# Kernel tuning notes

Measured on AMD Instinct MI355X. Metric: run time of the kernel, lower is better.

## Reference

```python
import jax, jax.numpy as jnp
import numpy as np

N = 65536      # num drones/nodes
E = 262144     # num directed edges
HID = 128      # hidden_dim
HEADS = 8      # gat1 heads
EPS = 1e-5


def _bn(x, g, b):
    # BatchNorm1d in training mode: batch statistics over dim 0 (biased var)
    mu = x.mean(0)
    var = ((x - mu) ** 2).mean(0)
    return (x - mu) * jax.lax.rsqrt(var + EPS) * g + b


def _gat(x, src, dst, W, a_src, a_dst, bias, heads, out_c, n, concat):
    # PyG GATConv math (self-loops already included in src/dst)
    xw = (x @ W).reshape(n, heads, out_c)               # [N,H,C]
    al_s = (xw * a_src).sum(-1)                          # [N,H]
    al_d = (xw * a_dst).sum(-1)                          # [N,H]
    e = jax.nn.leaky_relu(al_s[src] + al_d[dst], 0.2)    # [E',H]
    m = jax.ops.segment_max(e, dst, num_segments=n)      # stable softmax per target
    ex = jnp.exp(e - m[dst])
    den = jax.ops.segment_sum(ex, dst, num_segments=n)
    alpha = ex / den[dst]                                # [E',H]
    out = jax.ops.segment_sum(xw[src] * alpha[:, :, None], dst, num_segments=n)
    out = out.reshape(n, heads * out_c) if concat else out.mean(axis=1)
    return out + bias


def setup_inputs() -> dict:
    key = jax.random.key(0)
    ks = jax.random.split(key, 24)
    s = 0.05
    inp = {
        'node_features': jax.random.normal(ks[0], (N, HID), jnp.float32),
        'relative_poses': jax.random.normal(ks[1], (E, 6), jnp.float32),
        'pe_w1': jax.random.normal(ks[2], (6, 64), jnp.float32) * s,
        'pe_b1': jnp.zeros((64,), jnp.float32),
        'pe_g1': jnp.ones((64,), jnp.float32),
        'pe_be1': jnp.zeros((64,), jnp.float32),
        'pe_w2': jax.random.normal(ks[3], (64, HID), jnp.float32) * s,
        'pe_b2': jnp.zeros((HID,), jnp.float32),
        'pe_g2': jnp.ones((HID,), jnp.float32),
        'pe_be2': jnp.zeros((HID,), jnp.float32),
        'gamma_w': jax.random.normal(ks[4], (HID, HID), jnp.float32) * s,
        'gamma_b': jnp.zeros((HID,), jnp.float32),
        'beta_w': jax.random.normal(ks[5], (HID, HID), jnp.float32) * s,
        'beta_b': jnp.zeros((HID,), jnp.float32),
        'g1_w': jax.random.normal(ks[6], (HID, HEADS * HID), jnp.float32) * s,
        'g1_as': jax.random.normal(ks[7], (HEADS, HID), jnp.float32) * s,
        'g1_ad': jax.random.normal(ks[8], (HEADS, HID), jnp.float32) * s,
        'g1_b': jnp.zeros((HEADS * HID,), jnp.float32),
        'g2_w': jax.random.normal(ks[9], (HEADS * HID, HID), jnp.float32) * s,
        'g2_as': jax.random.normal(ks[10], (1, HID), jnp.float32) * s,
        'g2_ad': jax.random.normal(ks[11], (1, HID), jnp.float32) * s,
        'g2_b': jnp.zeros((HID,), jnp.float32),
        'edge_index': jax.random.randint(ks[12], (2, E), 0, N, jnp.int32),
    }
    return inp


def reference(node_features, relative_poses, pe_w1, pe_b1, pe_g1, pe_be1,
              pe_w2, pe_b2, pe_g2, pe_be2, gamma_w, gamma_b, beta_w, beta_b,
              g1_w, g1_as, g1_ad, g1_b, g2_w, g2_as, g2_ad, g2_b, edge_index):
    src, dst = edge_index[0], edge_index[1]
    # SpatialEncoding: pose MLP with training-mode BN, then FiLM modulation
    h = jax.nn.relu(_bn(relative_poses @ pe_w1 + pe_b1, pe_g1, pe_be1))
    h = jax.nn.relu(_bn(h @ pe_w2 + pe_b2, pe_g2, pe_be2))
    gamma = jax.nn.sigmoid(h @ gamma_w + gamma_b) * 2.0   # [E,HID]
    beta = h @ beta_w + beta_b
    modulated = gamma * node_features[src] + beta          # [E,HID]
    last = jnp.full((N,), -1, jnp.int32).at[dst].max(jnp.arange(E, dtype=jnp.int32))
    enc = jnp.where((last >= 0)[:, None], modulated[jnp.clip(last, 0)], node_features)
    # add self loops (PyG GATConv default)
    loops = jnp.arange(N, dtype=src.dtype)
    src_a = jnp.concatenate([src, loops])
    dst_a = jnp.concatenate([dst, loops])
    x = jax.nn.elu(_gat(enc, src_a, dst_a, g1_w, g1_as, g1_ad, g1_b, HEADS, HID, N, True))
    # dropout is identity in eval mode
    out = _gat(x, src_a, dst_a, g2_w, g2_as, g2_ad, g2_b, 1, HID, N, False)
    return out
```

## Files before the change

kernel.cpp:

```cpp
#include <hip/hip_runtime.h>
#include <hip/hip_bf16.h>
#include <math.h>

#define NN 65536
#define EE 262144

typedef unsigned short u16;
typedef unsigned int u32;
typedef __attribute__((ext_vector_type(8))) short bf16x8;
typedef __attribute__((ext_vector_type(4))) float f32x4;

__device__ __forceinline__ float bfu2f(u16 u){ return __uint_as_float(((u32)u)<<16); }
__device__ __forceinline__ u16 f2bfu(float f){
  u32 x = __float_as_uint(f);
  return (u16)((x + 0x7fffu + ((x>>16)&1u)) >> 16);
}
__device__ __forceinline__ float lrelu(float x){ return x>0.f ? x : 0.2f*x; }
__device__ __forceinline__ float fexp(float x){ return __expf(x); }

__global__ void k_cvtT(const float* __restrict__ B, u16* __restrict__ Bt, int K, int N){
  int idx = blockIdx.x*256+threadIdx.x;
  if (idx < K*N){ int k = idx/N, n = idx - k*N; Bt[n*K+k] = f2bfu(B[idx]); }
}

__global__ void k_cvtn(const float* __restrict__ nf, u16* __restrict__ nfb){
  int i = (blockIdx.x*256+threadIdx.x)*4;
  float4 v = *(const float4*)(nf + i);
  ushort4 o; o.x=f2bfu(v.x); o.y=f2bfu(v.y); o.z=f2bfu(v.z); o.w=f2bfu(v.w);
  *(ushort4*)(nfb + i) = o;
}

__global__ void k_bn1_stats(const float* __restrict__ poses, const float* __restrict__ w1,
                            const float* __restrict__ b1, float* __restrict__ sum1, float* __restrict__ sq1){
  int wave = (blockIdx.x*blockDim.x + threadIdx.x)>>6;
  int c = threadIdx.x & 63;
  float wc[6];
#pragma unroll
  for (int j=0;j<6;++j) wc[j] = w1[j*64+c];
  float bb = b1[c];
  float s=0.f,q=0.f;
  int e0 = wave*(EE/1024);
  for (int e=e0;e<e0+(EE/1024);++e){
    float z = bb;
#pragma unroll
    for (int j=0;j<6;++j) z = fmaf(poses[e*6+j], wc[j], z);
    s += z; q += z*z;
  }
  unsafeAtomicAdd(&sum1[c], s);
  unsafeAtomicAdd(&sq1[c], q);
}

__global__ void k_bn_fin(const float* __restrict__ sum, const float* __restrict__ sq,
                         const float* __restrict__ g, const float* __restrict__ be,
                         const float* __restrict__ bias0,
                         float* __restrict__ a, float* __restrict__ cc, int cols){
  int c = threadIdx.x;
  if (c<cols){
    float mu = sum[c]*(1.f/EE);
    float var = sq[c]*(1.f/EE) - mu*mu;
    float istd = rsqrtf(var + 1e-5f);
    float ac = istd*g[c];
    a[c] = ac;
    float cv = be[c] - mu*ac;
    if (bias0) cv += bias0[c]*ac;
    cc[c] = cv;
  }
}

__global__ void k_red2(const float* __restrict__ psum, const float* __restrict__ psq,
                       float* __restrict__ part2){
  int t = threadIdx.x;
  int b0 = blockIdx.x*128;
  float s = 0.f;
  if (t < 128){
    for (int k=0;k<128;++k) s += psum[(size_t)(b0+k)*128 + t];
  } else {
    int c = t-128;
    for (int k=0;k<128;++k) s += psq[(size_t)(b0+k)*128 + c];
  }
  part2[blockIdx.x*256 + t] = s;
}

__global__ void k_bn_fin2(const float* __restrict__ part2,
                          const float* __restrict__ g, const float* __restrict__ be,
                          const float* __restrict__ bias0,
                          float* __restrict__ a, float* __restrict__ cc){
  int c = threadIdx.x;
  if (c<128){
    float s=0.f,q=0.f;
    for (int k=0;k<32;++k){ s += part2[k*256+c]; q += part2[k*256+128+c]; }
    float mu = s*(1.f/EE);
    float var = q*(1.f/EE) - mu*mu;
    float istd = rsqrtf(var + 1e-5f);
    float ac = istd*g[c];
    a[c] = ac;
    cc[c] = be[c] - mu*ac + bias0[c]*ac;
  }
}

__global__ void k_h1(const float* __restrict__ poses, const float* __restrict__ w1, const float* __restrict__ b1,
                     const float* __restrict__ a1, const float* __restrict__ c1, u16* __restrict__ h1){
  int idx = blockIdx.x*256+threadIdx.x;
  int e = idx>>6, c = idx&63;
  float z = b1[c];
#pragma unroll
  for (int j=0;j<6;++j) z = fmaf(poses[e*6+j], w1[j*64+c], z);
  float h = z*a1[c]+c1[c];
  h1[idx] = f2bfu(h>0.f?h:0.f);
}

template<int EPI>
__launch_bounds__(256)
__global__ void k_mm(const u16* __restrict__ A, const u16* __restrict__ Bt,
                     const u16* __restrict__ Bt2,
                     int K, int lda, int ldbt, int ldc,
                     u16* __restrict__ outb,
                     const float* __restrict__ bias, const float* __restrict__ bias2,
                     float* __restrict__ ssum, float* __restrict__ ssq,
                     const float* __restrict__ gb,
                     const float* __restrict__ bb, const u16* __restrict__ nfselb,
                     const int* __restrict__ lastE){
  const int m0 = blockIdx.x*64, n0 = blockIdx.y*128;
  const int t = threadIdx.x;
  const int lane = t & 63, wv = t>>6;
  const int wr = wv>>1, wc = wv&1;
  __shared__ u16 Als[64*64];
  __shared__ u16 Bls[128*64];
  __shared__ u16 B2ls[EPI==7 ? 128*64 : 8];
  __shared__ float epiS[128][2];
  __shared__ float epiD[128][2];
  f32x4 acc[2][4];
  f32x4 acc2[2][4];
#pragma unroll
  for (int i=0;i<2;++i)
#pragma unroll
    for (int j=0;j<4;++j){ acc[i][j] = (f32x4){0.f,0.f,0.f,0.f}; acc2[i][j] = (f32x4){0.f,0.f,0.f,0.f}; }

  for (int k0=0;k0<K;k0+=64){
    constexpr int NS = (EPI==7) ? 10 : 6;
#pragma unroll
    for (int c=0;c<NS;++c){
      int gc = c*256 + t;
      if (gc < 512){
        int row = gc>>3, ch = gc&7;
        int sw = ((row<<3)|ch) ^ (row&7);
        *(uint4*)(Als + sw*8) = *(const uint4*)(A + (size_t)(m0+row)*lda + k0 + ch*8);
      } else if (gc < 1536){
        int g2 = gc - 512;
        int row = g2>>3, ch = g2&7;
        int sw = ((row<<3)|ch) ^ (row&7);
        *(uint4*)(Bls + sw*8) = *(const uint4*)(Bt + (size_t)(n0+row)*ldbt + k0 + ch*8);
      } else if constexpr (EPI==7){
        int g2 = gc - 1536;
        int row = g2>>3, ch = g2&7;
        int sw = ((row<<3)|ch) ^ (row&7);
        *(uint4*)(B2ls + sw*8) = *(const uint4*)(Bt2 + (size_t)(n0+row)*ldbt + k0 + ch*8);
      }
    }
    __syncthreads();
#pragma unroll
    for (int kk=0;kk<2;++kk){
      bf16x8 af[2], bfr[4];
      int ch = kk*4 + (lane>>4);
#pragma unroll
      for (int i=0;i<2;++i){
        int row = wr*32 + i*16 + (lane&15);
        int sw = ((row<<3)|ch) ^ (row&7);
        af[i] = *(const bf16x8*)(Als + sw*8);
      }
#pragma unroll
      for (int j=0;j<4;++j){
        int rowb = wc*64 + j*16 + (lane&15);
        int swb = ((rowb<<3)|ch) ^ (rowb&7);
        bfr[j] = *(const bf16x8*)(Bls + swb*8);
      }
#pragma unroll
      for (int i=0;i<2;++i)
#pragma unroll
        for (int j=0;j<4;++j)
          acc[i][j] = __builtin_amdgcn_mfma_f32_16x16x32_bf16(af[i], bfr[j], acc[i][j], 0,0,0);
      if constexpr (EPI==7){
        bf16x8 bf2[4];
#pragma unroll
        for (int j=0;j<4;++j){
          int rowb = wc*64 + j*16 + (lane&15);
          int swb = ((rowb<<3)|ch) ^ (rowb&7);
          bf2[j] = *(const bf16x8*)(B2ls + swb*8);
        }
#pragma unroll
        for (int i=0;i<2;++i)
#pragma unroll
          for (int j=0;j<4;++j)
            acc2[i][j] = __builtin_amdgcn_mfma_f32_16x16x32_bf16(af[i], bf2[j], acc2[i][j], 0,0,0);
      }
    }
    __syncthreads();
  }

  int cbase = wc*64 + (lane&15);

  if constexpr (EPI==6){
    float av[4], cv[4];
#pragma unroll
    for (int j=0;j<4;++j){ av[j]=bias[cbase+j*16]; cv[j]=bias2[cbase+j*16]; }
#pragma unroll
    for (int i=0;i<2;++i)
#pragma unroll
      for (int r=0;r<4;++r){
        int row = m0 + wr*32 + i*16 + ((lane>>4)<<2) + r;
#pragma unroll
        for (int j=0;j<4;++j){
          float h = fmaf(acc[i][j][r], av[j], cv[j]);
          outb[(size_t)row*128 + cbase + j*16] = f2bfu(h>0.f?h:0.f);
        }
      }
  } else if constexpr (EPI==2){
    float bv[4];
#pragma unroll
    for (int j=0;j<4;++j) bv[j]=bias[cbase+j*16];
    float s[4]={0,0,0,0}, q[4]={0,0,0,0};
#pragma unroll
    for (int i=0;i<2;++i)
#pragma unroll
      for (int j=0;j<4;++j)
#pragma unroll
        for (int r=0;r<4;++r){ float z = acc[i][j][r]+bv[j]; s[j]+=z; q[j]+=z*z; }
#pragma unroll
    for (int j=0;j<4;++j){
      float ss=s[j], qq=q[j];
      ss += __shfl_xor(ss,16); ss += __shfl_xor(ss,32);
      qq += __shfl_xor(qq,16); qq += __shfl_xor(qq,32);
      if (lane<16){
        epiS[wc*64+j*16+lane][wr] = ss;
        epiD[wc*64+j*16+lane][wr] = qq;
      }
    }
    __syncthreads();
    if (t<128){
      ssum[(size_t)blockIdx.x*128 + t] = epiS[t][0]+epiS[t][1];
      ssq[(size_t)blockIdx.x*128 + t]  = epiD[t][0]+epiD[t][1];
    }
  } else if constexpr (EPI==7){
    float gbv[4], bbv[4];
#pragma unroll
    for (int j=0;j<4;++j){ gbv[j]=gb[cbase+j*16]; bbv[j]=bb[cbase+j*16]; }
#pragma unroll
    for (int i=0;i<2;++i)
#pragma unroll
      for (int r=0;r<4;++r){
        int n = m0 + wr*32 + i*16 + ((lane>>4)<<2) + r;
        int le = lastE[n];
#pragma unroll
        for (int j=0;j<4;++j){
          int c = cbase + j*16;
          float nv = bfu2f(nfselb[(size_t)n*128+c]);
          float res;
          if (le>=0){
            float gp = acc[i][j][r] + gbv[j];
            float gam = 2.f/(1.f+fexp(-gp));
            res = fmaf(gam, nv, acc2[i][j][r] + bbv[j]);
          } else res = nv;
          outb[(size_t)n*128+c] = f2bfu(res);
        }
      }
  }
}

__launch_bounds__(512)
__global__ void k_proj(const u16* __restrict__ aggH, const u16* __restrict__ g1wt,
                       const u16* __restrict__ g2wt, const float* __restrict__ g1b,
                       const float* __restrict__ asv, const float* __restrict__ adv,
                       u16* __restrict__ xw2b, float* __restrict__ als2, float* __restrict__ ald2){
  const int m0 = blockIdx.x*64;
  const int t = threadIdx.x, lane = t&63, wv = t>>6;
  const int wr = wv>>1, wc = wv&1;
  __shared__ u16 ATls[64*128];
  __shared__ u16 Wls[128*64];
  __shared__ float epiS[64][2];
  __shared__ float epiD[64][2];
  const int cbase = wc*64 + (lane&15);
  f32x4 acc2[4];
#pragma unroll
  for (int j=0;j<4;++j) acc2[j] = (f32x4){0.f,0.f,0.f,0.f};

  for (int hh=0; hh<8; ++hh){
    f32x4 acc1[4];
#pragma unroll
    for (int j=0;j<4;++j) acc1[j] = (f32x4){0.f,0.f,0.f,0.f};

    for (int k0=0;k0<128;k0+=64){
#pragma unroll
      for (int c=0;c<3;++c){
        int gc = c*512 + t;
        if (gc < 512){
          int row = gc>>3, ch = gc&7;
          int sw = ((row<<3)|ch) ^ (row&7);
          *(uint4*)(ATls + sw*8) = *(const uint4*)(aggH + (size_t)(m0+row)*1024 + hh*128 + k0 + ch*8);
        } else {
          int g2 = gc - 512;
          int row = g2>>3, ch = g2&7;
          int sw = ((row<<3)|ch) ^ (row&7);
          *(uint4*)(Wls + sw*8) = *(const uint4*)(g1wt + (size_t)(hh*128+row)*128 + k0 + ch*8);
        }
      }
      __syncthreads();
      __builtin_amdgcn_s_setprio(1);
#pragma unroll
      for (int kk=0;kk<2;++kk){
        bf16x8 af, bfr[4];
        int ch = kk*4 + (lane>>4);
        {
          int row = wr*16 + (lane&15);
          int sw = ((row<<3)|ch) ^ (row&7);
          af = *(const bf16x8*)(ATls + sw*8);
        }
#pragma unroll
        for (int j=0;j<4;++j){
          int rowb = wc*64 + j*16 + (lane&15);
          int swb = ((rowb<<3)|ch) ^ (rowb&7);
          bfr[j] = *(const bf16x8*)(Wls + swb*8);
        }
#pragma unroll
        for (int j=0;j<4;++j)
          acc1[j] = __builtin_amdgcn_mfma_f32_16x16x32_bf16(af, bfr[j], acc1[j], 0,0,0);
      }
      __builtin_amdgcn_s_setprio(0);
      __syncthreads();
    }
    {
      float bv[4];
#pragma unroll
      for (int j=0;j<4;++j) bv[j] = g1b[hh*128 + cbase + j*16];
#pragma unroll
      for (int r=0;r<4;++r){
        int mrow = wr*16 + ((lane>>4)<<2) + r;
#pragma unroll
        for (int j=0;j<4;++j){
          int c = cbase + j*16;
          float v = acc1[j][r] + bv[j];
          v = v>0.f ? v : fexp(v)-1.f;
          int sw = ((mrow<<4)|(c>>3)) ^ (mrow&7);
          ATls[sw*8 + (c&7)] = f2bfu(v);
        }
      }
    }
    for (int k0=0;k0<128;k0+=64){
#pragma unroll
      for (int c=0;c<2;++c){
        int g2 = c*512 + t;
        int row = g2>>3, ch = g2&7;
        int sw = ((row<<3)|ch) ^ (row&7);
        *(uint4*)(Wls + sw*8) = *(const uint4*)(g2wt + (size_t)row*1024 + hh*128 + k0 + ch*8);
      }
      __syncthreads();
      __builtin_amdgcn_s_setprio(1);
#pragma unroll
      for (int kk=0;kk<2;++kk){
        bf16x8 af, bfr[4];
        int ch = kk*4 + (lane>>4);
        int chk = (k0>>3) + ch;
        {
          int row = wr*16 + (lane&15);
          int sw = ((row<<4)|chk) ^ (row&7);
          af = *(const bf16x8*)(ATls + sw*8);
        }
#pragma unroll
        for (int j=0;j<4;++j){
          int rowb = wc*64 + j*16 + (lane&15);
          int swb = ((rowb<<3)|ch) ^ (rowb&7);
          bfr[j] = *(const bf16x8*)(Wls + swb*8);
        }
#pragma unroll
        for (int j=0;j<4;++j)
          acc2[j] = __builtin_amdgcn_mfma_f32_16x16x32_bf16(af, bfr[j], acc2[j], 0,0,0);
      }
      __builtin_amdgcn_s_setprio(0);
      __syncthreads();
    }
  }
  float av[4], dv[4];
#pragma unroll
  for (int j=0;j<4;++j){ av[j]=asv[cbase+j*16]; dv[j]=adv[cbase+j*16]; }
#pragma unroll
  for (int r=0;r<4;++r){
    int lr = wr*16 + ((lane>>4)<<2) + r;
    int row = m0 + lr;
    float s=0.f, d=0.f;
#pragma unroll
    for (int j=0;j<4;++j){
      float v = acc2[j][r];
      xw2b[(size_t)row*128 + cbase + j*16] = f2bfu(v);
      s = fmaf(v, av[j], s); d = fmaf(v, dv[j], d);
    }
#pragma unroll
    for (int o=1;o<16;o<<=1){ s += __shfl_xor(s,o); d += __shfl_xor(d,o); }
    if ((lane&15)==0){ epiS[lr][wc]=s; epiD[lr][wc]=d; }
  }
  __syncthreads();
  if (t<64){
    als2[m0+t] = epiS[t][0]+epiS[t][1];
    ald2[m0+t] = epiD[t][0]+epiD[t][1];
  }
}

__global__ void k_lastdeg(const int* __restrict__ dst, int* __restrict__ lastE, int* __restrict__ deg){
  int e = blockIdx.x*256+threadIdx.x;
  int d = dst[e];
  atomicMax(&lastE[d], e);
  atomicAdd(&deg[d], 1);
}
__global__ void k_blocksum(const int* __restrict__ deg, int* __restrict__ bsum){
  __shared__ int s[256];
  int t = threadIdx.x;
  s[t] = deg[blockIdx.x*256+t];
  __syncthreads();
  for (int o=128;o>0;o>>=1){ if (t<o) s[t]+=s[t+o]; __syncthreads(); }
  if (!t) bsum[blockIdx.x]=s[0];
}
__global__ void k_scanb(int* __restrict__ bsum){
  __shared__ int s[256];
  int t=threadIdx.x;
  s[t]=bsum[t]; __syncthreads();
  for (int o=1;o<256;o<<=1){
    int v = s[t];
    if (t>=o) v += s[t-o];
    __syncthreads(); s[t]=v; __syncthreads();
  }
  bsum[t] = t ? s[t-1] : 0;
}
__global__ void k_indptr(const int* __restrict__ deg, const int* __restrict__ bsum, int* __restrict__ indptr){
  __shared__ int s[256];
  int t=threadIdx.x; int g=blockIdx.x*256+t;
  int d = deg[g];
  s[t]=d; __syncthreads();
  for (int o=1;o<256;o<<=1){
    int v = s[t];
    if (t>=o) v += s[t-o];
    __syncthreads(); s[t]=v; __syncthreads();
  }
  indptr[g] = bsum[blockIdx.x] + s[t] - d;
  if (g==NN-1) indptr[NN]=EE;
}
__global__ void k_fill(const int* __restrict__ srcA, const int* __restrict__ dstA,
                       const int* __restrict__ indptr, int* __restrict__ cursor, int* __restrict__ slist){
  int e = blockIdx.x*256+threadIdx.x;
  int d = dstA[e];
  int p = atomicAdd(&cursor[d],1);
  slist[indptr[d]+p] = srcA[e];
}

__global__ void k_gsel(const u16* __restrict__ h1, const u16* __restrict__ nodefb,
                       const int* __restrict__ lastE, const int* __restrict__ srcA,
                       u16* __restrict__ h1sel, u16* __restrict__ nfselb){
  int g = blockIdx.x*256+threadIdx.x;
  int n = g>>4, ch = g&15;
  int le = lastE[n];
  int src = (le>=0) ? srcA[le] : n;
  *(uint4*)(nfselb + (size_t)n*128 + ch*8) = *(const uint4*)(nodefb + (size_t)src*128 + ch*8);
  if (ch < 8){
    uint4 v = make_uint4(0,0,0,0);
    if (le>=0) v = *(const uint4*)(h1 + (size_t)le*64 + ch*8);
    *(uint4*)(h1sel + (size_t)n*64 + ch*8) = v;
  }
}

__global__ void k_vprep(const float* __restrict__ g1w, const float* __restrict__ as_,
                        const float* __restrict__ ad_, u16* __restrict__ vtb){
  int gid = blockIdx.x*256+threadIdx.x;
  if (gid<1024){
    int h = gid>>7, k = gid&127;
    float s=0.f,d=0.f;
    for (int cc=0;cc<128;++cc){
      float wv = g1w[(size_t)k*1024 + h*128+cc];
      s=fmaf(wv,as_[h*128+cc],s); d=fmaf(wv,ad_[h*128+cc],d);
    }
    vtb[h*128+k] = f2bfu(s);
    vtb[(h+8)*128+k] = f2bfu(d);
  }
}

__launch_bounds__(256)
__global__ void k_als1mm(const u16* __restrict__ encb, const u16* __restrict__ vtb,
                         float* __restrict__ als, float* __restrict__ ald){
  int t = threadIdx.x, lane = t&63, wv = t>>6;
  int m0 = blockIdx.x*64 + wv*16;
  f32x4 acc = (f32x4){0.f,0.f,0.f,0.f};
  const u16* arow = encb + (size_t)(m0 + (lane&15))*128;
  const u16* brow = vtb + (lane&15)*128;
  int ko = (lane>>4)*8;
#pragma unroll
  for (int k0=0;k0<128;k0+=32){
    bf16x8 af = *(const bf16x8*)(arow + k0 + ko);
    bf16x8 bf = *(const bf16x8*)(brow + k0 + ko);
    acc = __builtin_amdgcn_mfma_f32_16x16x32_bf16(af, bf, acc, 0,0,0);
  }
  int o = lane&15;
#pragma unroll
  for (int r=0;r<4;++r){
    int row = m0 + ((lane>>4)<<2) + r;
    if (o<8) als[(size_t)row*8+o] = acc[r];
    else     ald[(size_t)row*8+(o-8)] = acc[r];
  }
}

__launch_bounds__(256)
__global__ void k_soft1(const int* __restrict__ slist, const int* __restrict__ indptr,
                        const float* __restrict__ als, const float* __restrict__ ald,
                        float* __restrict__ wcsr, float* __restrict__ den1, float* __restrict__ wself1){
  int t = threadIdx.x;
  int n = blockIdx.x*4 + (t>>6);
  int lane = t&63;
  int ei = lane>>3, h = lane&7;
  int p0 = indptr[n], p1 = indptr[n+1];
  float adh = ald[(size_t)n*8+h];
  float selfsc = lrelu(als[(size_t)n*8+h] + adh);
  float m = selfsc;
  for (int p=p0+ei; p<p1; p+=8){
    int s = slist[p];
    m = fmaxf(m, lrelu(als[(size_t)s*8+h] + adh));
  }
  m = fmaxf(m, __shfl_xor(m,8));
  m = fmaxf(m, __shfl_xor(m,16));
  m = fmaxf(m, __shfl_xor(m,32));
  float ws = fexp(selfsc - m);
  float den = (ei==0) ? ws : 0.f;
  for (int p=p0+ei; p<p1; p+=8){
    int s = slist[p];
    float w = fexp(lrelu(als[(size_t)s*8+h] + adh) - m);
    wcsr[(size_t)p*8+h] = w;
    den += w;
  }
  den += __shfl_xor(den,8);
  den += __shfl_xor(den,16);
  den += __shfl_xor(den,32);
  if (ei==0){
    den1[(size_t)n*8+h] = den;
    wself1[(size_t)n*8+h] = ws;
  }
}

__launch_bounds__(256)
__global__ void k_soft2(const int* __restrict__ slist, const int* __restrict__ indptr,
                        const float* __restrict__ als, const float* __restrict__ ald,
                        float* __restrict__ wcsr, float* __restrict__ den2, float* __restrict__ wself2){
  int t = threadIdx.x;
  int n = blockIdx.x*16 + (t>>4);
  int l = t&15;
  int p0 = indptr[n], p1 = indptr[n+1];
  float adh = ald[n];
  float selfsc = lrelu(als[n] + adh);
  float m = selfsc;
  for (int p=p0+l; p<p1; p+=16)
    m = fmaxf(m, lrelu(als[slist[p]] + adh));
  m = fmaxf(m, __shfl_xor(m,1));
  m = fmaxf(m, __shfl_xor(m,2));
  m = fmaxf(m, __shfl_xor(m,4));
  m = fmaxf(m, __shfl_xor(m,8));
  float ws = fexp(selfsc - m);
  float den = (l==0) ? ws : 0.f;
  for (int p=p0+l; p<p1; p+=16){
    float w = fexp(lrelu(als[slist[p]] + adh) - m);
    wcsr[p] = w;
    den += w;
  }
  den += __shfl_xor(den,1);
  den += __shfl_xor(den,2);
  den += __shfl_xor(den,4);
  den += __shfl_xor(den,8);
  if (l==0){ den2[n] = den; wself2[n] = ws; }
}

__launch_bounds__(256)
__global__ void k_agg1(const u16* __restrict__ encb, const float* __restrict__ wcsr,
                       const float* __restrict__ den1, const float* __restrict__ wself1,
                       const int* __restrict__ slist, const int* __restrict__ indptr,
                       u16* __restrict__ aggH){
  int t = threadIdx.x;
  int n = blockIdx.x*4 + (t>>6);
  int lane = t&63;
  int c0 = lane*2;
  int p0 = indptr[n], p1 = indptr[n+1];
  float a0[8], a1[8];
  {
    ushort2 u = *(const ushort2*)(encb + (size_t)n*128 + c0);
    float x0 = bfu2f(u.x), x1 = bfu2f(u.y);
#pragma unroll
    for (int h=0;h<8;++h){
      float ws = wself1[(size_t)n*8 + h];
      a0[h] = ws*x0; a1[h] = ws*x1;
    }
  }
  for (int p=p0; p<p1; ++p){
    int s = slist[p];
    float4 w0 = *(const float4*)(wcsr + (size_t)p*8);
    float4 w1 = *(const float4*)(wcsr + (size_t)p*8 + 4);
    ushort2 u = *(const ushort2*)(encb + (size_t)s*128 + c0);
    float x0 = bfu2f(u.x), x1 = bfu2f(u.y);
    a0[0]=fmaf(w0.x,x0,a0[0]); a1[0]=fmaf(w0.x,x1,a1[0]);
    a0[1]=fmaf(w0.y,x0,a0[1]); a1[1]=fmaf(w0.y,x1,a1[1]);
    a0[2]=fmaf(w0.z,x0,a0[2]); a1[2]=fmaf(w0.z,x1,a1[2]);
    a0[3]=fmaf(w0.w,x0,a0[3]); a1[3]=fmaf(w0.w,x1,a1[3]);
    a0[4]=fmaf(w1.x,x0,a0[4]); a1[4]=fmaf(w1.x,x1,a1[4]);
    a0[5]=fmaf(w1.y,x0,a0[5]); a1[5]=fmaf(w1.y,x1,a1[5]);
    a0[6]=fmaf(w1.z,x0,a0[6]); a1[6]=fmaf(w1.z,x1,a1[6]);
    a0[7]=fmaf(w1.w,x0,a0[7]); a1[7]=fmaf(w1.w,x1,a1[7]);
  }
#pragma unroll
  for (int h=0;h<8;++h){
    float rr = 1.f/den1[(size_t)n*8 + h];
    u32 pk = (u32)f2bfu(a0[h]*rr) | ((u32)f2bfu(a1[h]*rr)<<16);
    *(u32*)(aggH + (size_t)n*1024 + h*128 + c0) = pk;
  }
}

__launch_bounds__(128)
__global__ void k_gat2(const u16* __restrict__ xw2b, const float* __restrict__ wcsr,
                       const float* __restrict__ den2, const float* __restrict__ wself2,
                       const int* __restrict__ slist, const int* __restrict__ indptr,
                       const float* __restrict__ g2b, float* __restrict__ out){
  int n = blockIdx.x, c = threadIdx.x;
  int p0 = indptr[n], p1 = indptr[n+1];
  float acc = wself2[n]*bfu2f(xw2b[(size_t)n*128+c]);
  int p = p0;
  for (; p+4<=p1; p+=4){
    int s0=slist[p], s1=slist[p+1], s2=slist[p+2], s3=slist[p+3];
    float w0=wcsr[p], w1=wcsr[p+1], w2=wcsr[p+2], w3=wcsr[p+3];
    float x0=bfu2f(xw2b[(size_t)s0*128+c]), x1=bfu2f(xw2b[(size_t)s1*128+c]);
    float x2=bfu2f(xw2b[(size_t)s2*128+c]), x3=bfu2f(xw2b[(size_t)s3*128+c]);
    acc = fmaf(w0,x0,acc); acc = fmaf(w1,x1,acc); acc = fmaf(w2,x2,acc); acc = fmaf(w3,x3,acc);
  }
  for (; p<p1; ++p){
    int s = slist[p];
    acc = fmaf(wcsr[p], bfu2f(xw2b[(size_t)s*128+c]), acc);
  }
  out[(size_t)n*128+c] = acc/den2[n] + g2b[c];
}

extern "C" void kernel_launch(void* const* d_in, const int* in_sizes, int n_in,
                              void* d_out, int out_size, void* d_ws, size_t ws_size,
                              hipStream_t stream){
  const float* nodef  = (const float*)d_in[0];
  const float* poses  = (const float*)d_in[1];
  const float* pe_w1  = (const float*)d_in[2];
  const float* pe_b1  = (const float*)d_in[3];
  const float* pe_g1  = (const float*)d_in[4];
  const float* pe_be1 = (const float*)d_in[5];
  const float* pe_w2  = (const float*)d_in[6];
  const float* pe_b2  = (const float*)d_in[7];
  const float* pe_g2  = (const float*)d_in[8];
  const float* pe_be2 = (const float*)d_in[9];
  const float* gamma_w= (const float*)d_in[10];
  const float* gamma_b= (const float*)d_in[11];
  const float* beta_w = (const float*)d_in[12];
  const float* beta_b = (const float*)d_in[13];
  const float* g1_w   = (const float*)d_in[14];
  const float* g1_as  = (const float*)d_in[15];
  const float* g1_ad  = (const float*)d_in[16];
  const float* g1_b   = (const float*)d_in[17];
  const float* g2_w   = (const float*)d_in[18];
  const float* g2_as  = (const float*)d_in[19];
  const float* g2_ad  = (const float*)d_in[20];
  const float* g2_b   = (const float*)d_in[21];
  const int*   eidx   = (const int*)d_in[22];
  const int* srcA = eidx;
  const int* dstA = eidx + EE;

  char* w = (char*)d_ws;
  const size_t MB = 1048576;
  u16*   aggH  = (u16*)(w + 0);
  u16*   h1    = (u16*)(w + 0);
  u16*   h1sel = (u16*)(w + 32*MB);
  u16*   h2b   = (u16*)(w + 40*MB);
  u16*   nodefb= (u16*)(w + 56*MB);
  u16*   nfselb= (u16*)(w + 72*MB);
  float* psum  = (float*)(w + 88*MB);
  float* psq   = (float*)(w + 90*MB);
  u16*   encb  = (u16*)(w + 128*MB);
  char* sm = w + 144*MB;
  size_t off = 0;
  auto alloc = [&](size_t b)->void*{ void* p = sm+off; off += (b+255)&~(size_t)255; return p; };
  u16* pe_w2t = (u16*)alloc(64*128*2);
  u16* gwt    = (u16*)alloc(128*128*2);
  u16* bwt    = (u16*)alloc(128*128*2);
  u16* g1wt   = (u16*)alloc(1024*128*2);
  u16* g2wt   = (u16*)alloc(128*1024*2);
  u16* vtb    = (u16*)alloc(16*128*2);
  float* part2 = (float*)alloc(32*256*4);
  float* als1  = (float*)alloc((size_t)NN*8*4);
  float* ald1  = (float*)alloc((size_t)NN*8*4);
  float* als2  = (float*)alloc((size_t)NN*4);
  float* ald2  = (float*)alloc((size_t)NN*4);
  float* wself1= (float*)alloc((size_t)NN*8*4);
  float* den1  = (float*)alloc((size_t)NN*8*4);
  float* wcsr1 = (float*)alloc((size_t)EE*8*4);
  float* wself2= (float*)alloc((size_t)NN*4);
  float* den2  = (float*)alloc((size_t)NN*4);
  float* wcsr2 = (float*)alloc((size_t)EE*4);
  u16*  xw2b   = (u16*)alloc((size_t)NN*128*2);
  int* lastE   = (int*)alloc((size_t)NN*4);
  int* deg     = (int*)alloc((size_t)NN*4);
  int* cursor  = (int*)alloc((size_t)NN*4);
  int* indptr  = (int*)alloc((size_t)(NN+1)*4);
  int* slist   = (int*)alloc((size_t)EE*4);
  int* bsum    = (int*)alloc(1024);
  float* stats = (float*)alloc(4096);
  float* sum1 = stats, *sq1 = stats+64;
  float* a1 = stats+384, *c1 = stats+448, *a2 = stats+512, *c2 = stats+640;

  hipMemsetAsync(stats, 0, 384*4, stream);
  hipMemsetAsync(deg, 0, (size_t)NN*4, stream);
  hipMemsetAsync(cursor, 0, (size_t)NN*4, stream);
  hipMemsetAsync(lastE, 0xFF, (size_t)NN*4, stream);

  k_cvtT<<<(64*128+255)/256,256,0,stream>>>(pe_w2, pe_w2t, 64, 128);
  k_cvtT<<<(128*128+255)/256,256,0,stream>>>(gamma_w, gwt, 128, 128);
  k_cvtT<<<(128*128+255)/256,256,0,stream>>>(beta_w, bwt, 128, 128);
  k_cvtT<<<(128*1024+255)/256,256,0,stream>>>(g1_w, g1wt, 128, 1024);
  k_cvtT<<<(1024*128+255)/256,256,0,stream>>>(g2_w, g2wt, 1024, 128);
  k_cvtn<<<NN*128/1024,256,0,stream>>>(nodef, nodefb);
  k_vprep<<<4,256,0,stream>>>(g1_w, g1_as, g1_ad, vtb);

  k_bn1_stats<<<256,256,0,stream>>>(poses, pe_w1, pe_b1, sum1, sq1);
  k_bn_fin<<<1,64,0,stream>>>(sum1, sq1, pe_g1, pe_be1, nullptr, a1, c1, 64);
  k_h1<<<65536,256,0,stream>>>(poses, pe_w1, pe_b1, a1, c1, h1);

  k_mm<2><<<dim3(4096,1),256,0,stream>>>(h1, pe_w2t, nullptr, 64, 64, 64, 0,
      nullptr, pe_b2, nullptr, psum, psq, nullptr, nullptr, nullptr, nullptr);
  k_red2<<<32,256,0,stream>>>(psum, psq, part2);
  k_bn_fin2<<<1,128,0,stream>>>(part2, pe_g2, pe_be2, pe_b2, a2, c2);

  k_lastdeg<<<1024,256,0,stream>>>(dstA, lastE, deg);
  k_blocksum<<<256,256,0,stream>>>(deg, bsum);
  k_scanb<<<1,256,0,stream>>>(bsum);
  k_indptr<<<256,256,0,stream>>>(deg, bsum, indptr);
  k_fill<<<1024,256,0,stream>>>(srcA, dstA, indptr, cursor, slist);

  k_gsel<<<4096,256,0,stream>>>(h1, nodefb, lastE, srcA, h1sel, nfselb);
  k_mm<6><<<dim3(1024,1),256,0,stream>>>(h1sel, pe_w2t, nullptr, 64, 64, 64, 128,
      h2b, a2, c2, nullptr, nullptr, nullptr, nullptr, nullptr, nullptr);

  k_mm<7><<<dim3(1024,1),256,0,stream>>>(h2b, gwt, bwt, 128, 128, 128, 128,
      encb, nullptr, nullptr, nullptr, nullptr, gamma_b, beta_b, nfselb, lastE);

  k_als1mm<<<1024,256,0,stream>>>(encb, vtb, als1, ald1);
  k_soft1<<<NN/4,256,0,stream>>>(slist, indptr, als1, ald1, wcsr1, den1, wself1);

  k_agg1<<<NN/4,256,0,stream>>>(encb, wcsr1, den1, wself1, slist, indptr, aggH);

  k_proj<<<1024,512,0,stream>>>(aggH, g1wt, g2wt, g1_b, g2_as, g2_ad, xw2b, als2, ald2);

  k_soft2<<<NN/16,256,0,stream>>>(slist, indptr, als2, ald2, wcsr2, den2, wself2);
  k_gat2<<<NN,128,0,stream>>>(xw2b, wcsr2, den2, wself2, slist, indptr, g2_b, (float*)d_out);
}
```

Before: 435.1 us.

## Merge prep kernels into one launch and vectorize h1 and GAT2 aggregation

Folds the weight transposes and conversions, the node-feature bf16 conversion, the vprep step, the BN1 statistics and the last-edge/degree pass into a single block-indexed k_prep launch, removing about eight small kernel launches and their serialization. k_h1 now computes two channels per thread and writes them with one 32-bit store. k_gat2 handles four nodes per 256-thread block, with each lane loading two bf16 values per neighbor and writing a float2. The trade-off is a heterogeneous kernel with unbalanced block work, plus less unrolling in the gat2 neighbor loop.

New measurement: 427.6 us. No clear change (-1.7%).

```diff
diff --git a/kernel.cpp b/kernel.cpp
--- a/kernel.cpp
+++ b/kernel.cpp
@@ -18,36 +18,79 @@
 __device__ __forceinline__ float lrelu(float x){ return x>0.f ? x : 0.2f*x; }
 __device__ __forceinline__ float fexp(float x){ return __expf(x); }
 
-__global__ void k_cvtT(const float* __restrict__ B, u16* __restrict__ Bt, int K, int N){
-  int idx = blockIdx.x*256+threadIdx.x;
-  if (idx < K*N){ int k = idx/N, n = idx - k*N; Bt[n*K+k] = f2bfu(B[idx]); }
-}
-
-__global__ void k_cvtn(const float* __restrict__ nf, u16* __restrict__ nfb){
-  int i = (blockIdx.x*256+threadIdx.x)*4;
-  float4 v = *(const float4*)(nf + i);
-  ushort4 o; o.x=f2bfu(v.x); o.y=f2bfu(v.y); o.z=f2bfu(v.z); o.w=f2bfu(v.w);
-  *(ushort4*)(nfb + i) = o;
-}
-
-__global__ void k_bn1_stats(const float* __restrict__ poses, const float* __restrict__ w1,
-                            const float* __restrict__ b1, float* __restrict__ sum1, float* __restrict__ sq1){
-  int wave = (blockIdx.x*blockDim.x + threadIdx.x)>>6;
-  int c = threadIdx.x & 63;
-  float wc[6];
-#pragma unroll
-  for (int j=0;j<6;++j) wc[j] = w1[j*64+c];
-  float bb = b1[c];
-  float s=0.f,q=0.f;
-  int e0 = wave*(EE/1024);
-  for (int e=e0;e<e0+(EE/1024);++e){
-    float z = bb;
-#pragma unroll
-    for (int j=0;j<6;++j) z = fmaf(poses[e*6+j], wc[j], z);
-    s += z; q += z*z;
-  }
-  unsafeAtomicAdd(&sum1[c], s);
-  unsafeAtomicAdd(&sq1[c], q);
+__global__ void k_prep(const float* __restrict__ nodef, u16* __restrict__ nodefb,
+                       const float* __restrict__ pe_w2, u16* __restrict__ pe_w2t,
+                       const float* __restrict__ gamma_w, u16* __restrict__ gwt,
+                       const float* __restrict__ beta_w, u16* __restrict__ bwt,
+                       const float* __restrict__ g1_w, u16* __restrict__ g1wt,
+                       const float* __restrict__ g2_w, u16* __restrict__ g2wt,
+                       const float* __restrict__ g1_as, const float* __restrict__ g1_ad,
+                       u16* __restrict__ vtb,
+                       const float* __restrict__ poses, const float* __restrict__ pe_w1,
+                       const float* __restrict__ pe_b1,
+                       float* __restrict__ sum1, float* __restrict__ sq1,
+                       const int* __restrict__ dstA, int* __restrict__ lastE, int* __restrict__ deg){
+  int bid = blockIdx.x, t = threadIdx.x;
+  if (bid < 8192){
+    int i = (bid*256+t)*4;
+    float4 v = *(const float4*)(nodef + i);
+    ushort4 o; o.x=f2bfu(v.x); o.y=f2bfu(v.y); o.z=f2bfu(v.z); o.w=f2bfu(v.w);
+    *(ushort4*)(nodefb + i) = o;
+  } else if (bid < 8224){
+    int idx = (bid-8192)*256+t;
+    int k = idx>>7, n = idx&127;
+    pe_w2t[n*64+k] = f2bfu(pe_w2[idx]);
+  } else if (bid < 8288){
+    int idx = (bid-8224)*256+t;
+    int k = idx>>7, n = idx&127;
+    gwt[n*128+k] = f2bfu(gamma_w[idx]);
+  } else if (bid < 8352){
+    int idx = (bid-8288)*256+t;
+    int k = idx>>7, n = idx&127;
+    bwt[n*128+k] = f2bfu(beta_w[idx]);
+  } else if (bid < 8864){
+    int idx = (bid-8352)*256+t;
+    int k = idx>>10, n = idx&1023;
+    g1wt[n*128+k] = f2bfu(g1_w[idx]);
+  } else if (bid < 9376){
+    int idx = (bid-8864)*256+t;
+    int k = idx>>7, n = idx&127;
+    g2wt[n*1024+k] = f2bfu(g2_w[idx]);
+  } else if (bid < 9380){
+    int gid = (bid-9376)*256+t;
+    if (gid<1024){
+      int h = gid>>7, k = gid&127;
+      float s=0.f,d=0.f;
+      for (int cc=0;cc<128;++cc){
+        float wv = g1_w[(size_t)k*1024 + h*128+cc];
+        s=fmaf(wv,g1_as[h*128+cc],s); d=fmaf(wv,g1_ad[h*128+cc],d);
+      }
+      vtb[h*128+k] = f2bfu(s);
+      vtb[(h+8)*128+k] = f2bfu(d);
+    }
+  } else if (bid < 9636){
+    int wave = ((bid-9380)*256 + t)>>6;
+    int c = t & 63;
+    float wc[6];
+#pragma unroll
+    for (int j=0;j<6;++j) wc[j] = pe_w1[j*64+c];
+    float bb = pe_b1[c];
+    float s=0.f,q=0.f;
+    int e0 = wave*(EE/1024);
+    for (int e=e0;e<e0+(EE/1024);++e){
+      float z = bb;
+#pragma unroll
+      for (int j=0;j<6;++j) z = fmaf(poses[e*6+j], wc[j], z);
+      s += z; q += z*z;
+    }
+    unsafeAtomicAdd(&sum1[c], s);
+    unsafeAtomicAdd(&sq1[c], q);
+  } else {
+    int e = (bid-9636)*256+t;
+    int d = dstA[e];
+    atomicMax(&lastE[d], e);
+    atomicAdd(&deg[d], 1);
+  }
 }
 
 __global__ void k_bn_fin(const float* __restrict__ sum, const float* __restrict__ sq,
@@ -101,12 +144,17 @@
 __global__ void k_h1(const float* __restrict__ poses, const float* __restrict__ w1, const float* __restrict__ b1,
                      const float* __restrict__ a1, const float* __restrict__ c1, u16* __restrict__ h1){
   int idx = blockIdx.x*256+threadIdx.x;
-  int e = idx>>6, c = idx&63;
-  float z = b1[c];
-#pragma unroll
-  for (int j=0;j<6;++j) z = fmaf(poses[e*6+j], w1[j*64+c], z);
-  float h = z*a1[c]+c1[c];
-  h1[idx] = f2bfu(h>0.f?h:0.f);
+  int e = idx>>5, cp = (idx&31)*2;
+  float z0 = b1[cp], z1 = b1[cp+1];
+#pragma unroll
+  for (int j=0;j<6;++j){
+    float pv = poses[e*6+j];
+    z0 = fmaf(pv, w1[j*64+cp], z0);
+    z1 = fmaf(pv, w1[j*64+cp+1], z1);
+  }
+  float h0 = z0*a1[cp]+c1[cp];     h0 = h0>0.f?h0:0.f;
+  float h1v = z1*a1[cp+1]+c1[cp+1]; h1v = h1v>0.f?h1v:0.f;
+  *(u32*)(h1 + (size_t)e*64 + cp) = (u32)f2bfu(h0) | ((u32)f2bfu(h1v)<<16);
 }
 
 template<int EPI>
@@ -403,12 +451,6 @@
   }
 }
 
-__global__ void k_lastdeg(const int* __restrict__ dst, int* __restrict__ lastE, int* __restrict__ deg){
-  int e = blockIdx.x*256+threadIdx.x;
-  int d = dst[e];
-  atomicMax(&lastE[d], e);
-  atomicAdd(&deg[d], 1);
-}
 __global__ void k_blocksum(const int* __restrict__ deg, int* __restrict__ bsum){
   __shared__ int s[256];
   int t = threadIdx.x;
@@ -461,21 +503,6 @@
     uint4 v = make_uint4(0,0,0,0);
     if (le>=0) v = *(const uint4*)(h1 + (size_t)le*64 + ch*8);
     *(uint4*)(h1sel + (size_t)n*64 + ch*8) = v;
-  }
-}
-
-__global__ void k_vprep(const float* __restrict__ g1w, const float* __restrict__ as_,
-                        const float* __restrict__ ad_, u16* __restrict__ vtb){
-  int gid = blockIdx.x*256+threadIdx.x;
-  if (gid<1024){
-    int h = gid>>7, k = gid&127;
-    float s=0.f,d=0.f;
-    for (int cc=0;cc<128;++cc){
-      float wv = g1w[(size_t)k*1024 + h*128+cc];
-      s=fmaf(wv,as_[h*128+cc],s); d=fmaf(wv,ad_[h*128+cc],d);
-    }
-    vtb[h*128+k] = f2bfu(s);
-    vtb[(h+8)*128+k] = f2bfu(d);
   }
 }
 
@@ -613,27 +640,39 @@
   }
 }
 
-__launch_bounds__(128)
+__launch_bounds__(256)
 __global__ void k_gat2(const u16* __restrict__ xw2b, const float* __restrict__ wcsr,
                        const float* __restrict__ den2, const float* __restrict__ wself2,
                        const int* __restrict__ slist, const int* __restrict__ indptr,
                        const float* __restrict__ g2b, float* __restrict__ out){
-  int n = blockIdx.x, c = threadIdx.x;
+  int t = threadIdx.x;
+  int n = blockIdx.x*4 + (t>>6);
+  int c0 = (t&63)*2;
   int p0 = indptr[n], p1 = indptr[n+1];
-  float acc = wself2[n]*bfu2f(xw2b[(size_t)n*128+c]);
+  float ws = wself2[n];
+  u32 u = *(const u32*)(xw2b + (size_t)n*128 + c0);
+  float a0 = ws*bfu2f((u16)u), a1 = ws*bfu2f((u16)(u>>16));
   int p = p0;
-  for (; p+4<=p1; p+=4){
-    int s0=slist[p], s1=slist[p+1], s2=slist[p+2], s3=slist[p+3];
-    float w0=wcsr[p], w1=wcsr[p+1], w2=wcsr[p+2], w3=wcsr[p+3];
-    float x0=bfu2f(xw2b[(size_t)s0*128+c]), x1=bfu2f(xw2b[(size_t)s1*128+c]);
-    float x2=bfu2f(xw2b[(size_t)s2*128+c]), x3=bfu2f(xw2b[(size_t)s3*128+c]);
-    acc = fmaf(w0,x0,acc); acc = fmaf(w1,x1,acc); acc = fmaf(w2,x2,acc); acc = fmaf(w3,x3,acc);
+  for (; p+2<=p1; p+=2){
+    int s0=slist[p], s1=slist[p+1];
+    float w0=wcsr[p], w1v=wcsr[p+1];
+    u32 v0 = *(const u32*)(xw2b + (size_t)s0*128 + c0);
+    u32 v1 = *(const u32*)(xw2b + (size_t)s1*128 + c0);
+    a0 = fmaf(w0, bfu2f((u16)v0), a0);       a1 = fmaf(w0, bfu2f((u16)(v0>>16)), a1);
+    a0 = fmaf(w1v, bfu2f((u16)v1), a0);      a1 = fmaf(w1v, bfu2f((u16)(v1>>16)), a1);
   }
   for (; p<p1; ++p){
     int s = slist[p];
-    acc = fmaf(wcsr[p], bfu2f(xw2b[(size_t)s*128+c]), acc);
-  }
-  out[(size_t)n*128+c] = acc/den2[n] + g2b[c];
+    float w = wcsr[p];
+    u32 v = *(const u32*)(xw2b + (size_t)s*128 + c0);
+    a0 = fmaf(w, bfu2f((u16)v), a0);
+    a1 = fmaf(w, bfu2f((u16)(v>>16)), a1);
+  }
+  float rr = 1.f/den2[n];
+  float2 o;
+  o.x = a0*rr + g2b[c0];
+  o.y = a1*rr + g2b[c0+1];
+  *(float2*)(out + (size_t)n*128 + c0) = o;
 }
 
 extern "C" void kernel_launch(void* const* d_in, const int* in_sizes, int n_in,
@@ -712,24 +751,18 @@
   hipMemsetAsync(cursor, 0, (size_t)NN*4, stream);
   hipMemsetAsync(lastE, 0xFF, (size_t)NN*4, stream);
 
-  k_cvtT<<<(64*128+255)/256,256,0,stream>>>(pe_w2, pe_w2t, 64, 128);
-  k_cvtT<<<(128*128+255)/256,256,0,stream>>>(gamma_w, gwt, 128, 128);
-  k_cvtT<<<(128*128+255)/256,256,0,stream>>>(beta_w, bwt, 128, 128);
-  k_cvtT<<<(128*1024+255)/256,256,0,stream>>>(g1_w, g1wt, 128, 1024);
-  k_cvtT<<<(1024*128+255)/256,256,0,stream>>>(g2_w, g2wt, 1024, 128);
-  k_cvtn<<<NN*128/1024,256,0,stream>>>(nodef, nodefb);
-  k_vprep<<<4,256,0,stream>>>(g1_w, g1_as, g1_ad, vtb);
-
-  k_bn1_stats<<<256,256,0,stream>>>(poses, pe_w1, pe_b1, sum1, sq1);
+  k_prep<<<10660,256,0,stream>>>(nodef, nodefb, pe_w2, pe_w2t, gamma_w, gwt, beta_w, bwt,
+                                 g1_w, g1wt, g2_w, g2wt, g1_as, g1_ad, vtb,
+                                 poses, pe_w1, pe_b1, sum1, sq1, dstA, lastE, deg);
+
   k_bn_fin<<<1,64,0,stream>>>(sum1, sq1, pe_g1, pe_be1, nullptr, a1, c1, 64);
-  k_h1<<<65536,256,0,stream>>>(poses, pe_w1, pe_b1, a1, c1, h1);
+  k_h1<<<32768,256,0,stream>>>(poses, pe_w1, pe_b1, a1, c1, h1);
 
   k_mm<2><<<dim3(4096,1),256,0,stream>>>(h1, pe_w2t, nullptr, 64, 64, 64, 0,
       nullptr, pe_b2, nullptr, psum, psq, nullptr, nullptr, nullptr, nullptr);
   k_red2<<<32,256,0,stream>>>(psum, psq, part2);
   k_bn_fin2<<<1,128,0,stream>>>(part2, pe_g2, pe_be2, pe_b2, a2, c2);
 
-  k_lastdeg<<<1024,256,0,stream>>>(dstA, lastE, deg);
   k_blocksum<<<256,256,0,stream>>>(deg, bsum);
   k_scanb<<<1,256,0,stream>>>(bsum);
   k_indptr<<<256,256,0,stream>>>(deg, bsum, indptr);
@@ -750,5 +783,5 @@
   k_proj<<<1024,512,0,stream>>>(aggH, g1wt, g2wt, g1_b, g2_as, g2_ad, xw2b, als2, ald2);
 
   k_soft2<<<NN/16,256,0,stream>>>(slist, indptr, als2, ald2, wcsr2, den2, wself2);
-  k_gat2<<<NN,128,0,stream>>>(xw2b, wcsr2, den2, wself2, slist, indptr, g2_b, (float*)d_out);
-}
+  k_gat2<<<NN/4,256,0,stream>>>(xw2b, wcsr2, den2, wself2, slist, indptr, g2_b, (float*)d_out);
+}
```
